# Kernel optimization log

Measured on AMD Instinct MI355X. Metric: run time of the kernel, lower is better.

## Reference

```python
import jax, jax.numpy as jnp
import numpy as np

B, P, E, D, A, M, V, T = 64, 196, 2048, 512, 512, 512, 10000, 31


def setup_inputs() -> dict:
    key = jax.random.key(0)
    ks = jax.random.split(key, 20)
    s = 0.02
    inp = {
        "encoder_out": jax.random.normal(ks[0], (B, P, E), jnp.float32),
        "captions": jax.random.randint(ks[1], (B, T), 0, V),
        "caption_lengths": jax.random.randint(ks[2], (B,), 2, T + 1).at[0].set(T),
        # parameters
        "W_emb": jax.random.normal(ks[3], (V, M), jnp.float32) * s,
        "We": jax.random.normal(ks[4], (A, E), jnp.float32) * s,
        "be": jnp.zeros((A,), jnp.float32),
        "Wd": jax.random.normal(ks[5], (A, D), jnp.float32) * s,
        "bd": jnp.zeros((A,), jnp.float32),
        "wf": jax.random.normal(ks[6], (1, A), jnp.float32) * s,
        "bf": jnp.zeros((1,), jnp.float32),
        "Wih": jax.random.normal(ks[7], (4 * D, M + E), jnp.float32) * s,
        "bih": jnp.zeros((4 * D,), jnp.float32),
        "Whh": jax.random.normal(ks[8], (4 * D, D), jnp.float32) * s,
        "bhh": jnp.zeros((4 * D,), jnp.float32),
        "Wfc": jax.random.normal(ks[9], (V, D), jnp.float32) * s,
        "bfc": jnp.zeros((V,), jnp.float32),
        "Wh0": jax.random.normal(ks[10], (D, E), jnp.float32) * s,
        "bh0": jnp.zeros((D,), jnp.float32),
        "Wc0": jax.random.normal(ks[11], (D, E), jnp.float32) * s,
        "bc0": jnp.zeros((D,), jnp.float32),
    }
    return inp


def _decode(encoder_out, W_emb, We, be, Wd, bd, wf, bf, Wih, bih, Whh, bhh,
            Wfc, bfc, Wh0, bh0, Wc0, bc0, captions, caption_lengths):
    # sort by length descending (matches torch .sort(descending=True))
    idx = jnp.argsort(-caption_lengths)
    lens = caption_lengths[idx]
    enc = encoder_out[idx]              # [B,P,E]
    caps = captions[idx]                # [B,T]
    emb = W_emb[caps]                   # [B,T,M]
    mean_enc = enc.mean(axis=1)         # [B,E]
    h0 = mean_enc @ Wh0.T + bh0         # [B,D]
    c0 = mean_enc @ Wc0.T + bc0
    dec_len = lens - 1                  # [B]
    att1 = enc @ We.T + be              # [B,P,A] precomputed encoder projection
    Tmax = caps.shape[1] - 1

    def step(carry, xs):
        h, c = carry
        e_t, t = xs                     # e_t: [B,M]
        active = (t < dec_len)          # [B]
        att2 = h @ Wd.T + bd            # [B,A]
        scores = jnp.tanh(att1 + att2[:, None, :]) @ wf[0] + bf[0]  # [B,P]
        alpha = jax.nn.softmax(scores, axis=-1)                      # [B,P]
        ctx = jnp.einsum('bp,bpe->be', alpha, enc)                   # [B,E]
        x = jnp.concatenate([e_t, ctx], axis=-1)                     # [B,M+E]
        gates = x @ Wih.T + bih + h @ Whh.T + bhh                    # [B,4D]
        i_g, f_g, g_g, o_g = jnp.split(gates, 4, axis=-1)
        c_t = jax.nn.sigmoid(f_g) * c + jax.nn.sigmoid(i_g) * jnp.tanh(g_g)
        h_t = jax.nn.sigmoid(o_g) * jnp.tanh(c_t)
        pred = h_t @ Wfc.T + bfc        # dropout in eval mode = identity
        m = active[:, None]
        h_new = jnp.where(m, h_t, h)
        c_new = jnp.where(m, c_t, c)
        pred = jnp.where(m, pred, 0.0)
        alpha = jnp.where(m, alpha, 0.0)
        return (h_new, c_new), (pred, alpha)

    emb_ts = jnp.swapaxes(emb[:, :Tmax, :], 0, 1)  # [Tmax,B,M]
    ts = jnp.arange(Tmax)
    _, (preds, alphas) = jax.lax.scan(step, (h0, c0), (emb_ts, ts))
    predictions = jnp.swapaxes(preds, 0, 1)   # [B,Tmax,V]
    alphas = jnp.swapaxes(alphas, 0, 1)       # [B,Tmax,P]
    return predictions, alphas


def reference(encoder_out, captions, caption_lengths, W_emb, We, be, Wd, bd,
              wf, bf, Wih, bih, Whh, bhh, Wfc, bfc, Wh0, bh0, Wc0, bc0):
    return _decode(encoder_out, W_emb, We, be, Wd, bd, wf, bf, Wih, bih,
                   Whh, bhh, Wfc, bfc, Wh0, bh0, Wc0, bc0,
                   captions, caption_lengths)
```

## Files before the change

kernel.cpp:

```cpp
#include <hip/hip_runtime.h>
#include <cstdint>
#include <cstddef>

typedef __attribute__((ext_vector_type(8))) short short8;
typedef __attribute__((ext_vector_type(4))) float f32x4;

#define DEV static __device__ __forceinline__

#define PRED_ELEMS 19200000ULL

#define OFF_ENC   0ULL
#define OFF_ATT1  51380224ULL
#define OFF_B1    64225280ULL
#define OFF_WFC   69468160ULL
#define OFF_WEB   79724544ULL
#define OFF_B0    81821696ULL
#define OFF_HH    81821696ULL
#define OFF_B2    86016000ULL
#define OFF_HX0   94404608ULL
#define OFF_HX1   94535680ULL
#define OFF_C     94666752ULL
#define OFF_CTX   94797824ULL
#define OFF_META  95059968ULL
#define OFF_ATT2  95125504ULL

DEV float b2f(unsigned short u){ unsigned v = ((unsigned)u) << 16; float f; __builtin_memcpy(&f, &v, 4); return f; }
DEV unsigned short f2b(float x){ unsigned v; __builtin_memcpy(&v, &x, 4); unsigned r = v + 0x7fffu + ((v >> 16) & 1u); return (unsigned short)(r >> 16); }
DEV float sigm(float x){ return 1.0f / (1.0f + __expf(-x)); }
DEV float tanhf_fast(float x){ float e = __expf(2.0f * x); return 1.0f - 2.0f / (e + 1.0f); }

DEV void gload16(const void* g, void* l){
  __builtin_amdgcn_global_load_lds((const __attribute__((address_space(1))) unsigned int*)g,
                                   (__attribute__((address_space(3))) unsigned int*)l, 16, 0, 0);
}

DEV void mm_core(const unsigned short* A, int ldA, int m0,
                 const unsigned short* Bm, int ldB, int n0,
                 int kIters, unsigned short* As, unsigned short* Bs, f32x4 acc[4])
{
  const int tid = threadIdx.x;
  const int lane = tid & 63, w = tid >> 6;
  const unsigned short* ga = A + (size_t)(m0 + lane) * ldA + w * 8;
  const unsigned short* gb = Bm + (size_t)(n0 + lane) * ldB + w * 8;
  unsigned short* la = As + w * 512;
  unsigned short* lb = Bs + w * 512;
  const int kb = lane >> 4, rr = lane & 15;
  for (int kk = 0; kk < kIters; ++kk) {
    gload16(ga, la); gload16(gb, lb);
    ga += 32; gb += 32;
    asm volatile("s_waitcnt vmcnt(0)" ::: "memory");
    __syncthreads();
    short8 bfr = *(const short8*)(Bs + (size_t)(kb * 64 + w * 16 + rr) * 8);
#pragma unroll
    for (int f = 0; f < 4; ++f) {
      short8 afr = *(const short8*)(As + (size_t)(kb * 64 + f * 16 + rr) * 8);
      acc[f] = __builtin_amdgcn_mfma_f32_16x16x32_bf16(afr, bfr, acc[f], 0, 0, 0);
    }
    __syncthreads();
  }
}

__global__ void k_meta(const int* __restrict__ caps, const int* __restrict__ lens, int* __restrict__ meta){
  int j = threadIdx.x;
  int lj = lens[j];
  int rank = 0;
  for (int k = 0; k < 64; ++k) { int lk = lens[k]; rank += (lk > lj) || (lk == lj && k < j); }
  meta[rank] = j; meta[64 + rank] = lj - 1;
  for (int t = 0; t < 31; ++t) meta[160 + rank * 31 + t] = caps[j * 31 + t];
  __syncthreads();
  if (j < 30) { int c = 0; for (int b = 0; b < 64; ++b) c += (meta[64 + b] > j); meta[128 + j] = c; }
}

__global__ __launch_bounds__(256) void k_encg(const float* __restrict__ enc, const int* __restrict__ meta, unsigned short* __restrict__ encb){
  int row = blockIdx.x; int b = row / 196, p = row % 196;
  const float* src = enc + ((size_t)meta[b] * 196 + p) * 2048;
  unsigned short* dst = encb + (size_t)row * 2048;
  int e0 = threadIdx.x * 8;
  short8 o;
#pragma unroll
  for (int j = 0; j < 8; ++j) o[j] = (short)f2b(src[e0 + j]);
  *(short8*)(dst + e0) = o;
}

__global__ __launch_bounds__(256) void k_wconv(const float* We, const float* Wh0, const float* Wc0,
                        const float* Wd, const float* Whh, const float* Wih, const float* Wfc,
                        unsigned short* Web, unsigned short* B0, unsigned short* B1,
                        unsigned short* Wfcb, unsigned short* B2){
  int bid = blockIdx.x, tid = threadIdx.x;
  if (bid < 512) {
    const float* s = We + (size_t)bid * 2048; unsigned short* d = Web + (size_t)bid * 2048;
    int e0 = tid * 8; short8 o;
#pragma unroll
    for (int j = 0; j < 8; ++j) o[j] = (short)f2b(s[e0 + j]);
    *(short8*)(d + e0) = o;
  } else if (bid < 1536) {
    int r = bid - 512;
    const float* s = (r < 512) ? (Wh0 + (size_t)r * 2048) : (Wc0 + (size_t)(r - 512) * 2048);
    unsigned short* d = B0 + (size_t)r * 2048;
    int e0 = tid * 8; short8 o;
#pragma unroll
    for (int j = 0; j < 8; ++j) o[j] = (short)f2b(s[e0 + j]);
    *(short8*)(d + e0) = o;
  } else if (bid < 3584) {
    int jr = bid - 1536; int g = (jr & 3) * 512 + (jr >> 2);
    const float* s = Wih + (size_t)g * 2560 + 512;
    unsigned short* d = B2 + (size_t)jr * 2048;
    int e0 = tid * 8; short8 o;
#pragma unroll
    for (int j = 0; j < 8; ++j) o[j] = (short)f2b(s[e0 + j]);
    *(short8*)(d + e0) = o;
  } else if (bid < 6144) {
    int n = bid - 3584; unsigned short* d = B1 + (size_t)n * 1024;
    int k0 = tid * 4;
    if (n < 512) {
#pragma unroll
      for (int j = 0; j < 4; ++j) { int k = k0 + j; d[k] = (k < 512) ? f2b(Wd[(size_t)n * 512 + k]) : (unsigned short)0; }
    } else {
      int j2 = n - 512; int g = (j2 & 3) * 512 + (j2 >> 2);
#pragma unroll
      for (int j = 0; j < 4; ++j) { int k = k0 + j;
        d[k] = (k < 512) ? f2b(Whh[(size_t)g * 512 + k]) : f2b(Wih[(size_t)g * 2560 + (k - 512)]); }
    }
  } else {
    int v = bid - 6144; unsigned short* d = Wfcb + (size_t)v * 512;
    int k0 = tid * 2;
#pragma unroll
    for (int j = 0; j < 2; ++j) d[k0 + j] = (v < 10000) ? f2b(Wfc[(size_t)v * 512 + k0 + j]) : (unsigned short)0;
  }
}

__global__ __launch_bounds__(256) void k_mean(const unsigned short* __restrict__ encb, unsigned short* __restrict__ meanb){
  int b = blockIdx.y, ch = blockIdx.x;
  int e = ch * 512 + threadIdx.x * 2;
  const unsigned short* ep = encb + (size_t)b * 196 * 2048 + e;
  float s0 = 0.f, s1 = 0.f;
  for (int p = 0; p < 196; ++p) {
    unsigned u = *(const unsigned*)(ep + (size_t)p * 2048);
    s0 += b2f((unsigned short)(u & 0xffff));
    s1 += b2f((unsigned short)(u >> 16));
  }
  const float inv = 1.0f / 196.0f;
  unsigned o = ((unsigned)f2b(s1 * inv) << 16) | f2b(s0 * inv);
  *(unsigned*)(meanb + (size_t)b * 2048 + e) = o;
}

__global__ __launch_bounds__(256) void k_h0c0(const unsigned short* meanb, const unsigned short* B0,
                      const float* bh0, const float* bc0, unsigned short* hx, float* cbuf){
  __shared__ __align__(16) unsigned short As[2048], Bs[2048];
  f32x4 acc[4];
#pragma unroll
  for (int f = 0; f < 4; ++f) acc[f] = (f32x4){0.f,0.f,0.f,0.f};
  int nt = blockIdx.x;
  mm_core(meanb, 2048, 0, B0, 2048, nt * 64, 64, As, Bs, acc);
  int lane = threadIdx.x & 63, w = threadIdx.x >> 6;
  int col = lane & 15, rhi = lane >> 4;
  int n = nt * 64 + w * 16 + col;
#pragma unroll
  for (int f = 0; f < 4; ++f)
#pragma unroll
    for (int r = 0; r < 4; ++r) {
      int b = f * 16 + rhi * 4 + r; float v = acc[f][r];
      if (n < 512) hx[(size_t)b * 1024 + n] = f2b(v + bh0[n]);
      else cbuf[(size_t)b * 512 + (n - 512)] = v + bc0[n - 512];
    }
}

__global__ void k_emb0(const float* __restrict__ Wemb, const int* __restrict__ meta, unsigned short* __restrict__ hx){
  int b = blockIdx.x;
  int cap = meta[160 + b * 31];
  for (int j = threadIdx.x; j < 512; j += 256)
    hx[(size_t)b * 1024 + 512 + j] = f2b(Wemb[(size_t)cap * 512 + j]);
}

__global__ __launch_bounds__(256) void k_att1(const unsigned short* __restrict__ encb,
                      const unsigned short* __restrict__ Web,
                      const float* __restrict__ be, unsigned short* __restrict__ att1b){
  __shared__ __align__(16) unsigned short As[2][4096], Bs[2][4096];
  int tid = threadIdx.x, lane = tid & 63, w = tid >> 6;
  int bid = blockIdx.x, mt, nt;
  if (bid < 384) { mt = (bid >> 5) * 8 + (bid & 7); nt = (bid >> 3) & 3; }
  else           { mt = 96 + ((bid - 384) >> 2);    nt = (bid - 384) & 3; }
  int wr = (w >> 1) * 64, wc = (w & 1) * 64;
  int rr = lane & 15, kb = lane >> 4;
  f32x4 acc[4][4];
#pragma unroll
  for (int f = 0; f < 4; ++f)
#pragma unroll
    for (int q = 0; q < 4; ++q) acc[f][q] = (f32x4){0.f,0.f,0.f,0.f};

  const unsigned short* gA = encb + (size_t)mt * 128 * 2048;
  const unsigned short* gB = Web + (size_t)nt * 128 * 2048;
  int L0 = tid, L1 = tid + 256;
  size_t s0 = (size_t)(L0 & 127) * 2048 + ((L0 >> 7) << 3);
  size_t s1 = (size_t)(L1 & 127) * 2048 + ((L1 >> 7) << 3);
  int d0 = (w * 64) * 8, d1 = (w * 64 + 256) * 8;

#define STAGE_A1(kk, bf) do { \
    gload16(gA + s0 + (size_t)(kk) * 32, &As[bf][d0]); \
    gload16(gB + s0 + (size_t)(kk) * 32, &Bs[bf][d0]); \
    gload16(gA + s1 + (size_t)(kk) * 32, &As[bf][d1]); \
    gload16(gB + s1 + (size_t)(kk) * 32, &Bs[bf][d1]); \
  } while (0)

  STAGE_A1(0, 0);
  __syncthreads();
  for (int kk = 0; kk < 64; ++kk) {
    int cur = kk & 1;
    if (kk < 63) STAGE_A1(kk + 1, cur ^ 1);
    short8 af[4], bq[4];
#pragma unroll
    for (int f = 0; f < 4; ++f)
      af[f] = *(const short8*)&As[cur][((kb << 7) + wr + f * 16 + rr) * 8];
#pragma unroll
    for (int q = 0; q < 4; ++q)
      bq[q] = *(const short8*)&Bs[cur][((kb << 7) + wc + q * 16 + rr) * 8];
#pragma unroll
    for (int f = 0; f < 4; ++f)
#pragma unroll
      for (int q = 0; q < 4; ++q)
        acc[f][q] = __builtin_amdgcn_mfma_f32_16x16x32_bf16(af[f], bq[q], acc[f][q], 0, 0, 0);
    __syncthreads();
  }
#undef STAGE_A1
  int col = lane & 15, rhi = lane >> 4;
#pragma unroll
  for (int q = 0; q < 4; ++q) {
    int n = nt * 128 + wc + q * 16 + col;
    float bev = be[n];
#pragma unroll
    for (int f = 0; f < 4; ++f)
#pragma unroll
      for (int r = 0; r < 4; ++r) {
        int m = mt * 128 + wr + f * 16 + rhi * 4 + r;
        att1b[(size_t)m * 512 + n] = f2b(acc[f][q][r] + bev);
      }
  }
}

__global__ __launch_bounds__(256) void k_att2(const unsigned short* __restrict__ hx,
                      const unsigned short* __restrict__ B1, const float* __restrict__ bd,
                      float* __restrict__ att2f){
  int w = threadIdx.x >> 6, lane = threadIdx.x & 63;
  int omega = blockIdx.x * 4 + w;
  int rr = lane & 15, kb8 = (lane >> 4) * 8;
  const unsigned short* pb = B1 + (size_t)(omega * 16 + rr) * 1024 + kb8;
  const unsigned short* pa0 = hx + (size_t)rr * 1024 + kb8;
  f32x4 acc[4];
#pragma unroll
  for (int f = 0; f < 4; ++f) acc[f] = (f32x4){0.f,0.f,0.f,0.f};
#pragma unroll 4
  for (int kk = 0; kk < 16; ++kk) {
    short8 bfr = *(const short8*)(pb + kk * 32);
#pragma unroll
    for (int f = 0; f < 4; ++f) {
      short8 afr = *(const short8*)(pa0 + (size_t)f * 16384 + kk * 32);
      acc[f] = __builtin_amdgcn_mfma_f32_16x16x32_bf16(afr, bfr, acc[f], 0, 0, 0);
    }
  }
  int col = lane & 15, rhi = lane >> 4;
  int n = omega * 16 + col; float bv = bd[n];
#pragma unroll
  for (int f = 0; f < 4; ++f)
#pragma unroll
    for (int r = 0; r < 4; ++r) { int b = f * 16 + rhi * 4 + r; att2f[(size_t)b * 512 + n] = acc[f][r] + bv; }
}

__global__ __launch_bounds__(1024) void k_sfc(int t, const float* __restrict__ att2f,
                      const unsigned short* __restrict__ att1b, const unsigned short* __restrict__ encb,
                      const float* __restrict__ wf, const float* __restrict__ bfp,
                      const int* __restrict__ meta, float* __restrict__ out, unsigned short* __restrict__ ctxb){
  int b = blockIdx.x;
  if (b >= meta[128 + t]) return;
  int tid = threadIdx.x, lane = tid & 63, wv = tid >> 6;
  __shared__ float sal[200];
  __shared__ float red[256];
  __shared__ float part[4][2048];

  {
    float wfr[8], a2[8];
#pragma unroll
    for (int j = 0; j < 8; ++j) { wfr[j] = wf[lane * 8 + j]; a2[j] = att2f[(size_t)b * 512 + lane * 8 + j]; }
    float bf0 = bfp[0];
    for (int i = 0; i < 13; ++i) {
      int p = i * 16 + wv;
      if (p < 196) {
        short8 av = *(const short8*)(att1b + ((size_t)(b * 196 + p)) * 512 + lane * 8);
        float s = 0.f;
#pragma unroll
        for (int j = 0; j < 8; ++j) s += tanhf_fast(b2f((unsigned short)av[j]) + a2[j]) * wfr[j];
#pragma unroll
        for (int off = 32; off; off >>= 1) s += __shfl_xor(s, off);
        if (lane == 0) sal[p] = s + bf0;
      }
    }
  }
  __syncthreads();

  float v = (tid < 196) ? sal[tid] : -3.0e38f;
  if (tid < 256) red[tid] = v;
  __syncthreads();
  for (int s = 128; s; s >>= 1) { if (tid < s) red[tid] = fmaxf(red[tid], red[tid + s]); __syncthreads(); }
  float mx = red[0]; __syncthreads();
  float ex = (tid < 196) ? __expf(v - mx) : 0.f;
  if (tid < 256) red[tid] = ex;
  __syncthreads();
  for (int s = 128; s; s >>= 1) { if (tid < s) red[tid] += red[tid + s]; __syncthreads(); }
  float inv = 1.0f / red[0];
  __syncthreads();
  if (tid < 196) {
    float al = ex * inv;
    sal[tid] = al;
    out[PRED_ELEMS + ((size_t)b * 30 + t) * 196 + tid] = al;
  }
  __syncthreads();

  {
    int rg = tid >> 8, cx = tid & 255;
    const unsigned short* ep = encb + (size_t)b * 196 * 2048 + cx * 8;
    float s8[8];
#pragma unroll
    for (int j = 0; j < 8; ++j) s8[j] = 0.f;
#pragma unroll 7
    for (int i = 0; i < 49; ++i) {
      int p = rg + i * 4;
      short8 vv = *(const short8*)(ep + (size_t)p * 2048);
      float a = sal[p];
#pragma unroll
      for (int j = 0; j < 8; ++j) s8[j] += a * b2f((unsigned short)vv[j]);
    }
#pragma unroll
    for (int j = 0; j < 8; ++j) part[rg][cx * 8 + j] = s8[j];
    __syncthreads();
    int ch2 = tid * 2;
    float r0 = part[0][ch2] + part[1][ch2] + part[2][ch2] + part[3][ch2];
    float r1 = part[0][ch2 + 1] + part[1][ch2 + 1] + part[2][ch2 + 1] + part[3][ch2 + 1];
    unsigned o = ((unsigned)f2b(r1) << 16) | f2b(r0);
    *(unsigned*)(ctxb + (size_t)b * 2048 + ch2) = o;
  }
}

__global__ __launch_bounds__(256) void k_sD(int t, const unsigned short* __restrict__ ctxb,
                       const unsigned short* __restrict__ hxc, unsigned short* __restrict__ hxn,
                       const unsigned short* __restrict__ B1, const unsigned short* __restrict__ B2,
                       const float* __restrict__ bih, const float* __restrict__ bhh,
                       const float* __restrict__ Wemb, const int* __restrict__ meta,
                       float* __restrict__ cbuf, unsigned short* __restrict__ hh){
  __shared__ float red[4][64][17];
  int w = threadIdx.x >> 6, lane = threadIdx.x & 63;
  int n0 = blockIdx.x * 16;
  int rr = lane & 15, kb8 = (lane >> 4) * 8;
  f32x4 acc[4];
#pragma unroll
  for (int f = 0; f < 4; ++f) acc[f] = (f32x4){0.f,0.f,0.f,0.f};
  {
    const unsigned short* pb = B2 + (size_t)(n0 + rr) * 2048 + w * 512 + kb8;
    const unsigned short* pa = ctxb + (size_t)rr * 2048 + w * 512 + kb8;
#pragma unroll 4
    for (int kk = 0; kk < 16; ++kk) {
      short8 bfr = *(const short8*)(pb + kk * 32);
#pragma unroll
      for (int f = 0; f < 4; ++f) {
        short8 afr = *(const short8*)(pa + (size_t)f * 32768 + kk * 32);
        acc[f] = __builtin_amdgcn_mfma_f32_16x16x32_bf16(afr, bfr, acc[f], 0, 0, 0);
      }
    }
  }
  {
    const unsigned short* pb = B1 + (size_t)(512 + n0 + rr) * 1024 + w * 256 + kb8;
    const unsigned short* pa = hxc + (size_t)rr * 1024 + w * 256 + kb8;
#pragma unroll 4
    for (int kk = 0; kk < 8; ++kk) {
      short8 bfr = *(const short8*)(pb + kk * 32);
#pragma unroll
      for (int f = 0; f < 4; ++f) {
        short8 afr = *(const short8*)(pa + (size_t)f * 16384 + kk * 32);
        acc[f] = __builtin_amdgcn_mfma_f32_16x16x32_bf16(afr, bfr, acc[f], 0, 0, 0);
      }
    }
  }
  int col = lane & 15, rhi = lane >> 4;
#pragma unroll
  for (int f = 0; f < 4; ++f)
#pragma unroll
    for (int r = 0; r < 4; ++r) red[w][f * 16 + rhi * 4 + r][col] = acc[f][r];
  __syncthreads();
  int b = threadIdx.x >> 2, dl = threadIdx.x & 3;
  int d = blockIdx.x * 4 + dl;
  float g4[4];
#pragma unroll
  for (int q = 0; q < 4; ++q) {
    int nl = dl * 4 + q;
    int j = n0 + nl;
    int g = (j & 3) * 512 + (j >> 2);
    g4[q] = red[0][b][nl] + red[1][b][nl] + red[2][b][nl] + red[3][b][nl] + bih[g] + bhh[g];
  }
  float c0 = cbuf[(size_t)b * 512 + d];
  float ct = sigm(g4[1]) * c0 + sigm(g4[0]) * tanhf_fast(g4[2]);
  float ht = sigm(g4[3]) * tanhf_fast(ct);
  int na = meta[128 + t];
  unsigned short hold = hxc[(size_t)b * 1024 + d];
  unsigned short hnew = (b < na) ? f2b(ht) : hold;
  if (b < na) cbuf[(size_t)b * 512 + d] = ct;
  hxn[(size_t)b * 1024 + d] = hnew;
  hh[((size_t)t * 64 + b) * 512 + d] = hnew;
  int cap = meta[160 + b * 31 + t + 1];
  hxn[(size_t)b * 1024 + 512 + d] = f2b(Wemb[(size_t)cap * 512 + d]);
}

__global__ __launch_bounds__(256) void k_pred(const unsigned short* __restrict__ hh,
                      const unsigned short* __restrict__ Wfcb, const float* __restrict__ bfc,
                      const int* __restrict__ meta, float* __restrict__ out){
  __shared__ __align__(16) unsigned short As[2][4096], Bs[2][4096];
  int tid = threadIdx.x, lane = tid & 63, w = tid >> 6;
  int mt = blockIdx.x % 15, nt = blockIdx.x / 15;
  int wr = (w >> 1) * 64, wc = (w & 1) * 64;
  int rr = lane & 15, kb = lane >> 4;
  f32x4 acc[4][4];
#pragma unroll
  for (int f = 0; f < 4; ++f)
#pragma unroll
    for (int q = 0; q < 4; ++q) acc[f][q] = (f32x4){0.f,0.f,0.f,0.f};

  const unsigned short* gA = hh + (size_t)mt * 128 * 512;
  int L0 = tid, L1 = tid + 256;
  size_t sa0 = (size_t)(L0 & 127) * 512 + ((L0 >> 7) << 3);
  size_t sa1 = (size_t)(L1 & 127) * 512 + ((L1 >> 7) << 3);
  int br0 = nt * 128 + (L0 & 127); if (br0 > 10015) br0 = 10015;
  int br1 = nt * 128 + (L1 & 127); if (br1 > 10015) br1 = 10015;
  size_t sb0 = (size_t)br0 * 512 + ((L0 >> 7) << 3);
  size_t sb1 = (size_t)br1 * 512 + ((L1 >> 7) << 3);
  int d0 = (w * 64) * 8, d1 = (w * 64 + 256) * 8;

#define STAGE_P(kk, bf) do { \
    gload16(gA + sa0 + (size_t)(kk) * 32, &As[bf][d0]); \
    gload16(Wfcb + sb0 + (size_t)(kk) * 32, &Bs[bf][d0]); \
    gload16(gA + sa1 + (size_t)(kk) * 32, &As[bf][d1]); \
    gload16(Wfcb + sb1 + (size_t)(kk) * 32, &Bs[bf][d1]); \
  } while (0)

  STAGE_P(0, 0);
  __syncthreads();
  for (int kk = 0; kk < 16; ++kk) {
    int cur = kk & 1;
    if (kk < 15) STAGE_P(kk + 1, cur ^ 1);
    short8 af[4], bq[4];
#pragma unroll
    for (int f = 0; f < 4; ++f)
      af[f] = *(const short8*)&As[cur][((kb << 7) + wr + f * 16 + rr) * 8];
#pragma unroll
    for (int q = 0; q < 4; ++q)
      bq[q] = *(const short8*)&Bs[cur][((kb << 7) + wc + q * 16 + rr) * 8];
#pragma unroll
    for (int f = 0; f < 4; ++f)
#pragma unroll
      for (int q = 0; q < 4; ++q)
        acc[f][q] = __builtin_amdgcn_mfma_f32_16x16x32_bf16(af[f], bq[q], acc[f][q], 0, 0, 0);
    __syncthreads();
  }
#undef STAGE_P
  int col = lane & 15, rhi = lane >> 4;
  int tt = mt * 2 + (wr >> 6);
  int na = meta[128 + tt];
#pragma unroll
  for (int q = 0; q < 4; ++q) {
    int n = nt * 128 + wc + q * 16 + col;
    if (n >= 10000) continue;
    float bv = bfc[n];
#pragma unroll
    for (int f = 0; f < 4; ++f)
#pragma unroll
      for (int r = 0; r < 4; ++r) {
        int b = f * 16 + rhi * 4 + r;
        if (b < na) out[(size_t)b * 300000 + (size_t)tt * 10000 + n] = acc[f][q][r] + bv;
      }
  }
}

extern "C" void kernel_launch(void* const* d_in, const int* in_sizes, int n_in,
                              void* d_out, int out_size, void* d_ws, size_t ws_size,
                              hipStream_t stream) {
  (void)in_sizes; (void)n_in; (void)ws_size;
  const float* enc  = (const float*)d_in[0];
  const int*   caps = (const int*)d_in[1];
  const int*   lens = (const int*)d_in[2];
  const float* Wemb = (const float*)d_in[3];
  const float* We   = (const float*)d_in[4];
  const float* be   = (const float*)d_in[5];
  const float* Wd   = (const float*)d_in[6];
  const float* bd   = (const float*)d_in[7];
  const float* wf   = (const float*)d_in[8];
  const float* bf   = (const float*)d_in[9];
  const float* Wih  = (const float*)d_in[10];
  const float* bih  = (const float*)d_in[11];
  const float* Whh  = (const float*)d_in[12];
  const float* bhh  = (const float*)d_in[13];
  const float* Wfc  = (const float*)d_in[14];
  const float* bfc  = (const float*)d_in[15];
  const float* Wh0  = (const float*)d_in[16];
  const float* bh0  = (const float*)d_in[17];
  const float* Wc0  = (const float*)d_in[18];
  const float* bc0  = (const float*)d_in[19];

  char* ws = (char*)d_ws;
  unsigned short* encb  = (unsigned short*)(ws + OFF_ENC);
  unsigned short* att1b = (unsigned short*)(ws + OFF_ATT1);
  unsigned short* B1    = (unsigned short*)(ws + OFF_B1);
  unsigned short* Wfcb  = (unsigned short*)(ws + OFF_WFC);
  unsigned short* Web   = (unsigned short*)(ws + OFF_WEB);
  unsigned short* B0    = (unsigned short*)(ws + OFF_B0);
  unsigned short* hh    = (unsigned short*)(ws + OFF_HH);
  unsigned short* B2    = (unsigned short*)(ws + OFF_B2);
  unsigned short* hx0   = (unsigned short*)(ws + OFF_HX0);
  unsigned short* hx1   = (unsigned short*)(ws + OFF_HX1);
  float*          cbuf  = (float*)(ws + OFF_C);
  unsigned short* ctxb  = (unsigned short*)(ws + OFF_CTX);
  int*            meta  = (int*)(ws + OFF_META);
  float*          att2f = (float*)(ws + OFF_ATT2);
  unsigned short* meanb = ctxb;
  float* out = (float*)d_out;

  hipMemsetAsync(d_out, 0, (size_t)out_size * sizeof(float), stream);
  k_meta<<<1, 64, 0, stream>>>(caps, lens, meta);
  k_encg<<<12544, 256, 0, stream>>>(enc, meta, encb);
  k_wconv<<<16160, 256, 0, stream>>>(We, Wh0, Wc0, Wd, Whh, Wih, Wfc, Web, B0, B1, Wfcb, B2);
  k_mean<<<dim3(4, 64), 256, 0, stream>>>(encb, meanb);
  k_h0c0<<<16, 256, 0, stream>>>(meanb, B0, bh0, bc0, hx0, cbuf);
  k_emb0<<<64, 256, 0, stream>>>(Wemb, meta, hx0);
  k_att1<<<392, 256, 0, stream>>>(encb, Web, be, att1b);
  for (int t = 0; t < 30; ++t) {
    unsigned short* hxc = (t & 1) ? hx1 : hx0;
    unsigned short* hxn = (t & 1) ? hx0 : hx1;
    k_att2<<<8, 256, 0, stream>>>(hxc, B1, bd, att2f);
    k_sfc<<<64, 1024, 0, stream>>>(t, att2f, att1b, encb, wf, bf, meta, out, ctxb);
    k_sD<<<128, 256, 0, stream>>>(t, ctxb, hxc, hxn, B1, B2, bih, bhh, Wemb, meta, cbuf, hh);
  }
  k_pred<<<1185, 256, 0, stream>>>(hh, Wfcb, bfc, meta, out);
}
```

Measured before the change: 2.031 ms.

## Split attention-context kernel across channel chunks to use more workgroups

Replaces the per-batch 1024-thread attention/context kernel with a 4x64 grid of 256-thread blocks, where each block handles one 512-channel slice of the context. Each block recomputes the attention scores and softmax for its batch row redundantly, and only channel block 0 writes alphas. This is meant to spread the per-step work over more CUs (256 blocks instead of 64) at the price of computing the score/softmax part four times.

```diff
diff --git a/kernel.cpp b/kernel.cpp
--- a/kernel.cpp
+++ b/kernel.cpp
@@ -265,77 +265,73 @@
     for (int r = 0; r < 4; ++r) { int b = f * 16 + rhi * 4 + r; att2f[(size_t)b * 512 + n] = acc[f][r] + bv; }
 }
 
-__global__ __launch_bounds__(1024) void k_sfc(int t, const float* __restrict__ att2f,
+__global__ __launch_bounds__(256) void k_sx(int t, const float* __restrict__ att2f,
                       const unsigned short* __restrict__ att1b, const unsigned short* __restrict__ encb,
                       const float* __restrict__ wf, const float* __restrict__ bfp,
                       const int* __restrict__ meta, float* __restrict__ out, unsigned short* __restrict__ ctxb){
-  int b = blockIdx.x;
+  int b = blockIdx.y, ch = blockIdx.x;
   if (b >= meta[128 + t]) return;
-  int tid = threadIdx.x, lane = tid & 63, wv = tid >> 6;
+  int tid = threadIdx.x, lane = tid & 63, w = tid >> 6;
   __shared__ float sal[200];
   __shared__ float red[256];
-  __shared__ float part[4][2048];
+  __shared__ float part[4][512];
 
   {
     float wfr[8], a2[8];
 #pragma unroll
     for (int j = 0; j < 8; ++j) { wfr[j] = wf[lane * 8 + j]; a2[j] = att2f[(size_t)b * 512 + lane * 8 + j]; }
     float bf0 = bfp[0];
-    for (int i = 0; i < 13; ++i) {
-      int p = i * 16 + wv;
-      if (p < 196) {
-        short8 av = *(const short8*)(att1b + ((size_t)(b * 196 + p)) * 512 + lane * 8);
-        float s = 0.f;
-#pragma unroll
-        for (int j = 0; j < 8; ++j) s += tanhf_fast(b2f((unsigned short)av[j]) + a2[j]) * wfr[j];
-#pragma unroll
-        for (int off = 32; off; off >>= 1) s += __shfl_xor(s, off);
-        if (lane == 0) sal[p] = s + bf0;
-      }
+    for (int i = 0; i < 49; ++i) {
+      int p = i * 4 + w;
+      short8 av = *(const short8*)(att1b + ((size_t)(b * 196 + p)) * 512 + lane * 8);
+      float s = 0.f;
+#pragma unroll
+      for (int j = 0; j < 8; ++j) s += tanhf_fast(b2f((unsigned short)av[j]) + a2[j]) * wfr[j];
+#pragma unroll
+      for (int off = 32; off; off >>= 1) s += __shfl_xor(s, off);
+      if (lane == 0) sal[p] = s + bf0;
     }
   }
   __syncthreads();
 
-  float v = (tid < 196) ? sal[tid] : -3.0e38f;
-  if (tid < 256) red[tid] = v;
+  {
+    float v = (tid < 196) ? sal[tid] : -3.0e38f;
+    red[tid] = v; __syncthreads();
+    for (int s = 128; s; s >>= 1) { if (tid < s) red[tid] = fmaxf(red[tid], red[tid + s]); __syncthreads(); }
+    float mx = red[0]; __syncthreads();
+    float ex = (tid < 196) ? __expf(v - mx) : 0.f;
+    red[tid] = ex; __syncthreads();
+    for (int s = 128; s; s >>= 1) { if (tid < s) red[tid] += red[tid + s]; __syncthreads(); }
+    float inv = 1.0f / red[0];
+    __syncthreads();
+    if (tid < 196) {
+      float al = ex * inv;
+      sal[tid] = al;
+      if (ch == 0) out[PRED_ELEMS + ((size_t)b * 30 + t) * 196 + tid] = al;
+    }
+  }
   __syncthreads();
-  for (int s = 128; s; s >>= 1) { if (tid < s) red[tid] = fmaxf(red[tid], red[tid + s]); __syncthreads(); }
-  float mx = red[0]; __syncthreads();
-  float ex = (tid < 196) ? __expf(v - mx) : 0.f;
-  if (tid < 256) red[tid] = ex;
-  __syncthreads();
-  for (int s = 128; s; s >>= 1) { if (tid < s) red[tid] += red[tid + s]; __syncthreads(); }
-  float inv = 1.0f / red[0];
-  __syncthreads();
-  if (tid < 196) {
-    float al = ex * inv;
-    sal[tid] = al;
-    out[PRED_ELEMS + ((size_t)b * 30 + t) * 196 + tid] = al;
-  }
-  __syncthreads();
 
   {
-    int rg = tid >> 8, cx = tid & 255;
-    const unsigned short* ep = encb + (size_t)b * 196 * 2048 + cx * 8;
+    const unsigned short* ep = encb + (size_t)b * 196 * 2048 + ch * 512 + lane * 8;
     float s8[8];
 #pragma unroll
     for (int j = 0; j < 8; ++j) s8[j] = 0.f;
 #pragma unroll 7
     for (int i = 0; i < 49; ++i) {
-      int p = rg + i * 4;
+      int p = w + i * 4;
       short8 vv = *(const short8*)(ep + (size_t)p * 2048);
       float a = sal[p];
 #pragma unroll
       for (int j = 0; j < 8; ++j) s8[j] += a * b2f((unsigned short)vv[j]);
     }
 #pragma unroll
-    for (int j = 0; j < 8; ++j) part[rg][cx * 8 + j] = s8[j];
+    for (int j = 0; j < 8; ++j) part[w][lane * 8 + j] = s8[j];
     __syncthreads();
-    int ch2 = tid * 2;
-    float r0 = part[0][ch2] + part[1][ch2] + part[2][ch2] + part[3][ch2];
-    float r1 = part[0][ch2 + 1] + part[1][ch2 + 1] + part[2][ch2 + 1] + part[3][ch2 + 1];
+    float r0 = part[0][tid * 2] + part[1][tid * 2] + part[2][tid * 2] + part[3][tid * 2];
+    float r1 = part[0][tid * 2 + 1] + part[1][tid * 2 + 1] + part[2][tid * 2 + 1] + part[3][tid * 2 + 1];
     unsigned o = ((unsigned)f2b(r1) << 16) | f2b(r0);
-    *(unsigned*)(ctxb + (size_t)b * 2048 + ch2) = o;
+    *(unsigned*)(ctxb + (size_t)b * 2048 + ch * 512 + tid * 2) = o;
   }
 }
 
@@ -531,7 +527,7 @@
     unsigned short* hxc = (t & 1) ? hx1 : hx0;
     unsigned short* hxn = (t & 1) ? hx0 : hx1;
     k_att2<<<8, 256, 0, stream>>>(hxc, B1, bd, att2f);
-    k_sfc<<<64, 1024, 0, stream>>>(t, att2f, att1b, encb, wf, bf, meta, out, ctxb);
+    k_sx<<<dim3(4, 64), 256, 0, stream>>>(t, att2f, att1b, encb, wf, bf, meta, out, ctxb);
     k_sD<<<128, 256, 0, stream>>>(t, ctxb, hxc, hxn, B1, B2, bih, bhh, Wemb, meta, cbuf, hh);
   }
   k_pred<<<1185, 256, 0, stream>>>(hh, Wfcb, bfc, meta, out);
```

After: 2.470 ms. 1.22x slower.
